# Kernel tuning notes

Hardware: AMD Instinct MI355X
Metric: run time of the kernel (lower is better)

Reference implementation:

```python
import jax, jax.numpy as jnp
import numpy as np

B, C, H, W = 8, 256, 64, 64
C8 = C // 8


def setup_inputs() -> dict:
    key = jax.random.key(0)
    ks = jax.random.split(key, 8)
    x = jax.random.normal(ks[0], (B, C, H, W), dtype=jnp.float32)
    # 1x1 convs == channel matmuls; store as [out_ch, in_ch] plus bias
    Wq = jax.random.normal(ks[1], (C8, C), dtype=jnp.float32) * (1.0 / np.sqrt(C))
    bq = jnp.zeros((C8,), dtype=jnp.float32)
    Wk = jax.random.normal(ks[2], (C8, C), dtype=jnp.float32) * (1.0 / np.sqrt(C))
    bk = jnp.zeros((C8,), dtype=jnp.float32)
    Wv = jax.random.normal(ks[3], (C, C), dtype=jnp.float32) * (1.0 / np.sqrt(C))
    bv = jnp.zeros((C,), dtype=jnp.float32)
    # gamma initialized to zero in the module, but use a nonzero value so the
    # attention branch actually contributes to the output being checked
    gamma = jnp.full((1,), 0.5, dtype=jnp.float32)
    return {"x": x, "Wq": Wq, "bq": bq, "Wk": Wk, "bk": bk, "Wv": Wv, "bv": bv, "gamma": gamma}


def reference(x, Wq, bq, Wk, bk, Wv, bv, gamma):
    b, c, h, w = x.shape
    n = h * w
    xf = x.reshape(b, c, n)                                  # [B, C, N]
    q = jnp.einsum('oc,bcn->bon', Wq, xf) + bq[None, :, None]  # [B, C8, N]
    k = jnp.einsum('oc,bcn->bon', Wk, xf) + bk[None, :, None]  # [B, C8, N]
    v = jnp.einsum('oc,bcn->bon', Wv, xf) + bv[None, :, None]  # [B, C,  N]
    # attention[b, i, j] = sum_d q[b, d, i] * k[b, d, j]  (no 1/sqrt(d) scaling!)
    scores = jnp.einsum('bdi,bdj->bij', q, k)                # [B, N, N]
    attn = jax.nn.softmax(scores, axis=-1)                   # softmax over j
    # out[b, c, i] = sum_j v[b, c, j] * attn[b, i, j]
    out = jnp.einsum('bcj,bij->bci', v, attn)                # [B, C, N]
    out = out.reshape(b, c, h, w)
    return gamma[0] * out + x
```

## Files before the change

### kernel.cpp

```cpp
#include <hip/hip_runtime.h>
#include <math.h>

#define BB 8
#define CC 256
#define NN 4096

typedef float f4 __attribute__((ext_vector_type(4)));
typedef short bh8 __attribute__((ext_vector_type(8)));

__device__ __forceinline__ unsigned short f2bf(float f) {
    unsigned u = __builtin_bit_cast(unsigned, f);
    u += 0x7fff + ((u >> 16) & 1);
    return (unsigned short)(u >> 16);
}
__device__ __forceinline__ unsigned packbf(float a, float b) {
    return (unsigned)f2bf(a) | ((unsigned)f2bf(b) << 16);
}

__device__ __forceinline__ float exp2_fast(float x) {
    float r;
    asm("v_exp_f32 %0, %1" : "=v"(r) : "v"(x));
    return r;
}

__global__ void prep_w_kernel(const float* __restrict__ Wq, const float* __restrict__ bq,
                              const float* __restrict__ Wk, const float* __restrict__ bk,
                              const float* __restrict__ Wv, const float* __restrict__ bv,
                              unsigned short* __restrict__ Whi, unsigned short* __restrict__ Wlo,
                              float* __restrict__ bcat) {
    const float L2E = 1.4426950408889634f;
    int idx = blockIdx.x * 256 + threadIdx.x;
    if (idx < 320) {
        bcat[idx] = (idx < 32) ? bq[idx] * L2E : (idx < 64 ? bk[idx - 32] : bv[idx - 64]);
    }
    if (idx < 320 * 256) {
        int o = idx >> 8;
        int c = idx & 255;
        float v = (o < 32) ? Wq[o * 256 + c] * L2E
                           : (o < 64 ? Wk[(o - 32) * 256 + c] : Wv[(o - 64) * 256 + c]);
        unsigned short hi = f2bf(v);
        float vhi = __builtin_bit_cast(float, ((unsigned)hi) << 16);
        Whi[idx] = hi;
        Wlo[idx] = f2bf(v - vhi);
    }
}

__global__ __launch_bounds__(256, 2) void qkv_kernel(
    const float* __restrict__ x, const unsigned short* __restrict__ Whi,
    const unsigned short* __restrict__ Wlo, const float* __restrict__ bcat,
    unsigned short* __restrict__ q64, unsigned short* __restrict__ k64,
    unsigned short* __restrict__ vC) {
    __shared__ __align__(16) char smem[67584];
    unsigned short* xsTh = (unsigned short*)smem;
    unsigned short* xsTl = (unsigned short*)(smem + 33792);
    unsigned short* qkl = (unsigned short*)smem;
    unsigned short* vsl = (unsigned short*)(smem + 16384);

    int blk = blockIdx.x;
    int b = blk >> 6;
    int i0 = (blk & 63) << 6;
    int t = threadIdx.x;
    const float* xb = x + ((size_t)b << 20);

    for (int idx = t; idx < 256 * 64; idx += 256) {
        int c = idx >> 6, ii = idx & 63;
        float v = xb[((size_t)c << 12) + i0 + ii];
        unsigned short hi = f2bf(v);
        float vhi = __builtin_bit_cast(float, ((unsigned)hi) << 16);
        xsTh[ii * 264 + c] = hi;
        xsTl[ii * 264 + c] = f2bf(v - vhi);
    }
    __syncthreads();

    int lane = t & 63;
    int w = t >> 6;
    int g = lane >> 4;
    int li = lane & 15;

    f4 acc[5][4];
#pragma unroll
    for (int tt = 0; tt < 5; ++tt)
#pragma unroll
        for (int it = 0; it < 4; ++it) acc[tt][it] = (f4){0.f, 0.f, 0.f, 0.f};

#pragma unroll
    for (int tt = 0; tt < 5; ++tt) {
        int ot = w + 4 * tt;
        bool qk = (ot < 4);
        const unsigned short* wrh = Whi + (size_t)(16 * ot + li) * 256 + 8 * g;
        const unsigned short* wrl = Wlo + (size_t)(16 * ot + li) * 256 + 8 * g;
        bh8 ah[8], al[8];
#pragma unroll
        for (int ck = 0; ck < 8; ++ck) {
            ah[ck] = *(const bh8*)(wrh + 32 * ck);
            al[ck] = *(const bh8*)(wrl + 32 * ck);
        }
#pragma unroll
        for (int it = 0; it < 4; ++it) {
            const unsigned short* xrh = xsTh + (16 * it + li) * 264 + 8 * g;
            const unsigned short* xrl = xsTl + (16 * it + li) * 264 + 8 * g;
            f4 a = acc[tt][it];
            if (qk) {
#pragma unroll
                for (int ck = 0; ck < 8; ++ck) {
                    bh8 xh = *(const bh8*)(xrh + 32 * ck);
                    bh8 xl = *(const bh8*)(xrl + 32 * ck);
                    a = __builtin_amdgcn_mfma_f32_16x16x32_bf16(ah[ck], xh, a, 0, 0, 0);
                    a = __builtin_amdgcn_mfma_f32_16x16x32_bf16(al[ck], xh, a, 0, 0, 0);
                    a = __builtin_amdgcn_mfma_f32_16x16x32_bf16(ah[ck], xl, a, 0, 0, 0);
                }
            } else {
#pragma unroll
                for (int ck = 0; ck < 8; ++ck) {
                    bh8 xh = *(const bh8*)(xrh + 32 * ck);
                    a = __builtin_amdgcn_mfma_f32_16x16x32_bf16(ah[ck], xh, a, 0, 0, 0);
                    a = __builtin_amdgcn_mfma_f32_16x16x32_bf16(al[ck], xh, a, 0, 0, 0);
                }
            }
            acc[tt][it] = a;
        }
    }
    __syncthreads();

#pragma unroll
    for (int tt = 0; tt < 5; ++tt) {
        int ot = w + 4 * tt;
        float bias[4];
#pragma unroll
        for (int e = 0; e < 4; ++e) bias[e] = bcat[16 * ot + 4 * g + e];
#pragma unroll
        for (int it = 0; it < 4; ++it) {
            int ii = 16 * it + li;
#pragma unroll
            for (int e = 0; e < 4; ++e) {
                int o = 16 * ot + 4 * g + e;
                float v = acc[tt][it][e] + bias[e];
                if (o < 64) {
                    unsigned short hi = f2bf(v);
                    float vhi = __builtin_bit_cast(float, ((unsigned)hi) << 16);
                    unsigned short lo = f2bf(v - vhi);
                    if (o < 32) {
                        qkl[ii * 128 + o] = hi;
                        qkl[ii * 128 + 32 + o] = lo;
                    } else {
                        qkl[ii * 128 + 32 + o] = hi;
                        qkl[ii * 128 + 64 + o] = lo;
                    }
                } else {
                    vsl[(o - 64) * 66 + ii] = f2bf(v);
                }
            }
        }
    }
    __syncthreads();

    const unsigned* qk32 = (const unsigned*)qkl;
    unsigned* qb = (unsigned*)(q64 + ((size_t)(b * NN + i0)) * 64);
    unsigned* kb = (unsigned*)(k64 + ((size_t)(b * NN + i0)) * 64);
    for (int idx = t; idx < 64 * 32; idx += 256) {
        int row = idx >> 5, dw = idx & 31;
        qb[row * 32 + dw] = qk32[row * 64 + dw];
        kb[row * 32 + dw] = qk32[row * 64 + 32 + dw];
    }
    for (int idx = t; idx < 256 * 32; idx += 256) {
        int c = idx >> 5, dw = idx & 31;
        unsigned val = *(const unsigned*)(vsl + c * 66 + 2 * dw);
        int i = 2 * dw;
        int p = 32 * (i >> 5) + 8 * ((i >> 2) & 3) + 4 * ((i >> 4) & 1) + (i & 3);
        *(unsigned*)(vC + ((size_t)(b * CC + c)) * NN + i0 + p) = val;
    }
}

__global__ __launch_bounds__(256, 2) void attn_kernel(
    const unsigned short* __restrict__ q64, const unsigned short* __restrict__ k64,
    const unsigned short* __restrict__ vC, const float* __restrict__ x,
    const float* __restrict__ gamma, float* __restrict__ out) {
    __shared__ unsigned short vs[2][256 * 64];

    int t = threadIdx.x;
    int lane = t & 63;
    int w = t >> 6;
    int g = lane >> 4;
    int li = lane & 15;
    int blk = blockIdx.x;
    int b = blk & 7;
    int i0 = (blk >> 3) << 6;
    int qb = i0 + 16 * w;

    const unsigned short* vb = vC + ((size_t)b * CC) * NN;
    const unsigned short* kb = k64 + ((size_t)b * NN) * 64;

    bh8 qf[2];
#pragma unroll
    for (int s = 0; s < 2; ++s)
        qf[s] = *(const bh8*)(q64 + ((size_t)(b * NN + qb + li)) * 64 + s * 32 + 8 * g);

    const unsigned short* vsrcb[8];
#pragma unroll
    for (int s = 0; s < 8; ++s) {
        int c = 64 * w + 8 * s + (lane >> 3);
        int slot = (lane & 7) ^ (c & 7);
        vsrcb[s] = vb + (size_t)c * NN + slot * 8;
    }
    const unsigned short* ksrcb[8];
#pragma unroll
    for (int jt = 0; jt < 4; ++jt)
#pragma unroll
        for (int s = 0; s < 2; ++s)
            ksrcb[jt * 2 + s] = kb + (size_t)(16 * jt + li) * 64 + s * 32 + 8 * g;

    f4 acc[16];
#pragma unroll
    for (int ct = 0; ct < 16; ++ct) acc[ct] = (f4){0.f, 0.f, 0.f, 0.f};
    float m = -INFINITY, l = 0.f;

    auto stageV = [&](int buf, int j0) {
#pragma unroll
        for (int s = 0; s < 8; ++s) {
            __builtin_amdgcn_global_load_lds(
                (const __attribute__((address_space(1))) unsigned int*)(vsrcb[s] + j0),
                (__attribute__((address_space(3))) unsigned int*)(&vs[buf][(64 * w + 8 * s) * 64]),
                16, 0, 0);
        }
    };
    auto loadK = [&](bh8 (&kf)[4][2], int j0) {
        size_t joff = (size_t)j0 * 64;
#pragma unroll
        for (int jt = 0; jt < 4; ++jt)
#pragma unroll
            for (int s = 0; s < 2; ++s)
                kf[jt][s] = *(const bh8*)(ksrcb[jt * 2 + s] + joff);
    };
    auto qkComp = [&](f4 (&sOut)[4], bh8 (&kc)[4][2]) {
#pragma unroll
        for (int jt = 0; jt < 4; ++jt) {
            f4 a = {0.f, 0.f, 0.f, 0.f};
            a = __builtin_amdgcn_mfma_f32_16x16x32_bf16(kc[jt][0], qf[0], a, 0, 0, 0);
            a = __builtin_amdgcn_mfma_f32_16x16x32_bf16(kc[jt][1], qf[0], a, 0, 0, 0);
            a = __builtin_amdgcn_mfma_f32_16x16x32_bf16(kc[jt][0], qf[1], a, 0, 0, 0);
            sOut[jt] = a;
        }
    };

    bh8 kf0[4][2], kf1[4][2];
    f4 sA[4], sB[4];

    stageV(0, 0);
    loadK(kf0, 0);
    loadK(kf1, 64);
    qkComp(sA, kf0);
    __syncthreads();

    auto step = [&](int tt, bh8 (&kNext)[4][2], bh8 (&kLoad)[4][2],
                    f4 (&sCur)[4], f4 (&sNxt)[4], int buf) {
        if (tt < 63) stageV(buf ^ 1, (tt + 1) << 6);
        if (tt < 62) loadK(kLoad, (tt + 2) << 6);

        if (tt < 63) qkComp(sNxt, kNext);

        float mx = sCur[0][0];
#pragma unroll
        for (int jt = 0; jt < 4; ++jt)
#pragma unroll
            for (int e = 0; e < 4; ++e) mx = fmaxf(mx, sCur[jt][e]);
        if (!__all(mx <= m + 11.541561f)) {
            mx = fmaxf(mx, __shfl_xor(mx, 16));
            mx = fmaxf(mx, __shfl_xor(mx, 32));
            float mnew = fmaxf(m, mx);
            float sc = exp2_fast(m - mnew);
            l *= sc;
#pragma unroll
            for (int ct = 0; ct < 16; ++ct)
#pragma unroll
                for (int e = 0; e < 4; ++e) acc[ct][e] *= sc;
            m = mnew;
        }
        float sum = 0.f;
#pragma unroll
        for (int jt = 0; jt < 4; ++jt)
#pragma unroll
            for (int e = 0; e < 4; ++e) {
                float p = exp2_fast(sCur[jt][e] - m);
                sCur[jt][e] = p;
                sum += p;
            }
        l += sum;

        const char* vsb = (const char*)vs[buf];
#pragma unroll
        for (int h = 0; h < 2; ++h) {
            union { unsigned u[4]; bh8 v; } pf;
            pf.u[0] = packbf(sCur[2 * h + 0][0], sCur[2 * h + 0][1]);
            pf.u[1] = packbf(sCur[2 * h + 0][2], sCur[2 * h + 0][3]);
            pf.u[2] = packbf(sCur[2 * h + 1][0], sCur[2 * h + 1][1]);
            pf.u[3] = packbf(sCur[2 * h + 1][2], sCur[2 * h + 1][3]);
            bh8 pb = pf.v;
            __builtin_amdgcn_s_setprio(1);
#pragma unroll
            for (int ct = 0; ct < 16; ++ct) {
                int c = 16 * ct + li;
                int off = c * 128 + ((64 * h + 16 * g) ^ ((c & 7) << 4));
                bh8 vf = *(const bh8*)(vsb + off);
                acc[ct] = __builtin_amdgcn_mfma_f32_16x16x32_bf16(vf, pb, acc[ct], 0, 0, 0);
            }
            __builtin_amdgcn_s_setprio(0);
        }
        __syncthreads();
    };

    for (int tt = 0; tt < 64; tt += 2) {
        step(tt, kf1, kf0, sA, sB, 0);
        step(tt + 1, kf0, kf1, sB, sA, 1);
    }

    l += __shfl_xor(l, 16);
    l += __shfl_xor(l, 32);

    float gm = gamma[0];
    float rl = 1.f / l;
    const float* xb = x + ((size_t)b * CC) * NN;
    float* ob = out + ((size_t)b * CC) * NN;
    int i = qb + li;
#pragma unroll
    for (int ct = 0; ct < 16; ++ct)
#pragma unroll
        for (int e = 0; e < 4; ++e) {
            int c = 16 * ct + 4 * g + e;
            size_t idx = (size_t)c * NN + i;
            ob[idx] = gm * (acc[ct][e] * rl) + xb[idx];
        }
}

extern "C" void kernel_launch(void* const* d_in, const int* in_sizes, int n_in,
                              void* d_out, int out_size, void* d_ws, size_t ws_size,
                              hipStream_t stream) {
    const float* x = (const float*)d_in[0];
    const float* Wq = (const float*)d_in[1];
    const float* bq = (const float*)d_in[2];
    const float* Wk = (const float*)d_in[3];
    const float* bk = (const float*)d_in[4];
    const float* Wv = (const float*)d_in[5];
    const float* bv = (const float*)d_in[6];
    const float* gamma = (const float*)d_in[7];
    float* out = (float*)d_out;

    unsigned short* ws16 = (unsigned short*)d_ws;
    unsigned short* q64w = ws16;
    unsigned short* k64w = ws16 + 2097152;
    unsigned short* vCw = ws16 + 4194304;
    unsigned short* Whiw = ws16 + 12582912;
    unsigned short* Wlow = Whiw + 81920;
    float* bcatw = (float*)(Wlow + 81920);

    prep_w_kernel<<<320, 256, 0, stream>>>(Wq, bq, Wk, bk, Wv, bv, Whiw, Wlow, bcatw);
    qkv_kernel<<<BB * (NN / 64), 256, 0, stream>>>(x, Whiw, Wlow, bcatw, q64w, k64w, vCw);
    attn_kernel<<<512, 256, 0, stream>>>(q64w, k64w, vCw, x, gamma, out);
}
```

Measured before the change: 205.5 us.

## Pipeline softmax one tile ahead so exp work overlaps PV MFMAs

Moves the softmax of the next tile (max, exp, bf16 pack) ahead of the current tile's P·V MFMA loop. Probabilities are carried between iterations as packed bf16 registers instead of fp32 scores, and the accumulator rescale is applied after the current tile's MFMAs. The goal is to let VALU exp and pack work overlap with matrix-core work and to shorten the dependency chain before the MFMAs. Ordering is still correct because the current P was computed with the old max and the rescale is applied afterwards, but the reordering may shift register pressure.

```diff
diff --git a/kernel.cpp b/kernel.cpp
--- a/kernel.cpp
+++ b/kernel.cpp
@@ -212,7 +212,7 @@
     f4 acc[16];
 #pragma unroll
     for (int ct = 0; ct < 16; ++ct) acc[ct] = (f4){0.f, 0.f, 0.f, 0.f};
-    float m = -INFINITY, l = 0.f;
+    float m, l;
 
     auto stageV = [&](int buf, int j0) {
 #pragma unroll
@@ -241,76 +241,114 @@
             sOut[jt] = a;
         }
     };
+    auto packP = [&](f4 (&sT)[4], bh8 (&pN)[2]) {
+        union { unsigned u[4]; bh8 v; } pf0, pf1;
+        pf0.u[0] = packbf(sT[0][0], sT[0][1]);
+        pf0.u[1] = packbf(sT[0][2], sT[0][3]);
+        pf0.u[2] = packbf(sT[1][0], sT[1][1]);
+        pf0.u[3] = packbf(sT[1][2], sT[1][3]);
+        pf1.u[0] = packbf(sT[2][0], sT[2][1]);
+        pf1.u[1] = packbf(sT[2][2], sT[2][3]);
+        pf1.u[2] = packbf(sT[3][0], sT[3][1]);
+        pf1.u[3] = packbf(sT[3][2], sT[3][3]);
+        pN[0] = pf0.v;
+        pN[1] = pf1.v;
+    };
 
     bh8 kf0[4][2], kf1[4][2];
-    f4 sA[4], sB[4];
+    bh8 P0[2], P1[2];
 
     stageV(0, 0);
     loadK(kf0, 0);
     loadK(kf1, 64);
-    qkComp(sA, kf0);
+    {
+        f4 sT[4];
+        qkComp(sT, kf0);
+        float mx = sT[0][0];
+#pragma unroll
+        for (int jt = 0; jt < 4; ++jt)
+#pragma unroll
+            for (int e = 0; e < 4; ++e) mx = fmaxf(mx, sT[jt][e]);
+        mx = fmaxf(mx, __shfl_xor(mx, 16));
+        mx = fmaxf(mx, __shfl_xor(mx, 32));
+        m = mx;
+        float sum = 0.f;
+#pragma unroll
+        for (int jt = 0; jt < 4; ++jt)
+#pragma unroll
+            for (int e = 0; e < 4; ++e) {
+                float p = exp2_fast(sT[jt][e] - m);
+                sT[jt][e] = p;
+                sum += p;
+            }
+        l = sum;
+        packP(sT, P0);
+    }
     __syncthreads();
 
     auto step = [&](int tt, bh8 (&kNext)[4][2], bh8 (&kLoad)[4][2],
-                    f4 (&sCur)[4], f4 (&sNxt)[4], int buf) {
+                    bh8 (&pC)[2], bh8 (&pN)[2], int buf) {
         if (tt < 63) stageV(buf ^ 1, (tt + 1) << 6);
         if (tt < 62) loadK(kLoad, (tt + 2) << 6);
 
-        if (tt < 63) qkComp(sNxt, kNext);
-
-        float mx = sCur[0][0];
-#pragma unroll
-        for (int jt = 0; jt < 4; ++jt)
-#pragma unroll
-            for (int e = 0; e < 4; ++e) mx = fmaxf(mx, sCur[jt][e]);
-        if (!__all(mx <= m + 11.541561f)) {
-            mx = fmaxf(mx, __shfl_xor(mx, 16));
-            mx = fmaxf(mx, __shfl_xor(mx, 32));
-            float mnew = fmaxf(m, mx);
-            float sc = exp2_fast(m - mnew);
-            l *= sc;
-#pragma unroll
-            for (int ct = 0; ct < 16; ++ct)
-#pragma unroll
-                for (int e = 0; e < 4; ++e) acc[ct][e] *= sc;
-            m = mnew;
-        }
-        float sum = 0.f;
-#pragma unroll
-        for (int jt = 0; jt < 4; ++jt)
-#pragma unroll
-            for (int e = 0; e < 4; ++e) {
-                float p = exp2_fast(sCur[jt][e] - m);
-                sCur[jt][e] = p;
-                sum += p;
-            }
-        l += sum;
+        bool resc = false;
+        float sc = 1.f;
+        if (tt < 63) {
+            f4 sT[4];
+            qkComp(sT, kNext);
+            float mx = sT[0][0];
+#pragma unroll
+            for (int jt = 0; jt < 4; ++jt)
+#pragma unroll
+                for (int e = 0; e < 4; ++e) mx = fmaxf(mx, sT[jt][e]);
+            if (!__all(mx <= m + 11.541561f)) {
+                mx = fmaxf(mx, __shfl_xor(mx, 16));
+                mx = fmaxf(mx, __shfl_xor(mx, 32));
+                float mnew = fmaxf(m, mx);
+                sc = exp2_fast(m - mnew);
+                l *= sc;
+                m = mnew;
+                resc = true;
+            }
+            float sum = 0.f;
+#pragma unroll
+            for (int jt = 0; jt < 4; ++jt)
+#pragma unroll
+                for (int e = 0; e < 4; ++e) {
+                    float p = exp2_fast(sT[jt][e] - m);
+                    sT[jt][e] = p;
+                    sum += p;
+                }
+            l += sum;
+            packP(sT, pN);
+        }
 
         const char* vsb = (const char*)vs[buf];
+        __builtin_amdgcn_s_setprio(1);
 #pragma unroll
         for (int h = 0; h < 2; ++h) {
-            union { unsigned u[4]; bh8 v; } pf;
-            pf.u[0] = packbf(sCur[2 * h + 0][0], sCur[2 * h + 0][1]);
-            pf.u[1] = packbf(sCur[2 * h + 0][2], sCur[2 * h + 0][3]);
-            pf.u[2] = packbf(sCur[2 * h + 1][0], sCur[2 * h + 1][1]);
-            pf.u[3] = packbf(sCur[2 * h + 1][2], sCur[2 * h + 1][3]);
-            bh8 pb = pf.v;
-            __builtin_amdgcn_s_setprio(1);
 #pragma unroll
             for (int ct = 0; ct < 16; ++ct) {
                 int c = 16 * ct + li;
                 int off = c * 128 + ((64 * h + 16 * g) ^ ((c & 7) << 4));
                 bh8 vf = *(const bh8*)(vsb + off);
-                acc[ct] = __builtin_amdgcn_mfma_f32_16x16x32_bf16(vf, pb, acc[ct], 0, 0, 0);
-            }
-            __builtin_amdgcn_s_setprio(0);
+                acc[ct] = __builtin_amdgcn_mfma_f32_16x16x32_bf16(vf, pC[h], acc[ct], 0, 0, 0);
+            }
+        }
+        __builtin_amdgcn_s_setprio(0);
+
+        if (resc) {
+#pragma unroll
+            for (int ct = 0; ct < 16; ++ct)
+#pragma unroll
+                for (int e = 0; e < 4; ++e) acc[ct][e] *= sc;
         }
         __syncthreads();
     };
 
     for (int tt = 0; tt < 64; tt += 2) {
-        step(tt, kf1, kf0, sA, sB, 0);
-        step(tt + 1, kf0, kf1, sB, sA, 1);
+        step(tt, kf1, kf0, P0, P1, 0);
+        step(tt + 1, kf0, kf1, P1, P0, 1);
     }
 
     l += __shfl_xor(l, 16);
```

Measured after the change: 207.0 us. About the same (+0.8%).
